# Kernel tuning notes

Measured on AMD Instinct MI355X. Metric: run time of the kernel, lower is better.

## Reference

```python
import jax, jax.numpy as jnp
import numpy as np

N_NODES = 100000
N_EDGES = 1600000
NUM_FEATURES = 128
HIDDEN_DIM = 64
NUM_CLASSES = 2
NUM_GRAPHS = 128


def setup_inputs() -> dict:
    key = jax.random.key(0)
    ks = jax.random.split(key, 9)
    x = jax.random.normal(ks[0], (N_NODES, NUM_FEATURES), dtype=jnp.float32)
    edge_index = jax.random.randint(ks[1], (2, N_EDGES), 0, N_NODES, dtype=jnp.int64)
    batch = jnp.sort(jax.random.randint(ks[2], (N_NODES,), 0, NUM_GRAPHS, dtype=jnp.int64))
    # GCNConv weights (PyG: glorot-init linear, zero bias; values here arbitrary for a numeric baseline)
    s1 = 1.0 / np.sqrt(NUM_FEATURES)
    s2 = 1.0 / np.sqrt(HIDDEN_DIM)
    W1 = jax.random.uniform(ks[3], (NUM_FEATURES, HIDDEN_DIM), jnp.float32, -s1, s1)
    b1 = jax.random.uniform(ks[4], (HIDDEN_DIM,), jnp.float32, -s1, s1)
    W2 = jax.random.uniform(ks[5], (HIDDEN_DIM, HIDDEN_DIM), jnp.float32, -s2, s2)
    b2 = jax.random.uniform(ks[6], (HIDDEN_DIM,), jnp.float32, -s2, s2)
    Wf = jax.random.uniform(ks[7], (HIDDEN_DIM, NUM_CLASSES), jnp.float32, -s2, s2)
    bf = jax.random.uniform(ks[8], (NUM_CLASSES,), jnp.float32, -s2, s2)
    return {"x": x, "edge_index": edge_index, "batch": batch,
            "W1": W1, "b1": b1, "W2": W2, "b2": b2, "Wf": Wf, "bf": bf}


def _gcn_aggregate(h, src, dst, norm, n_nodes):
    # messages: gather source features, scale by sym-norm coefficient, scatter-add at targets
    msg = h[src] * norm[:, None]                       # [E+N, F]
    return jax.ops.segment_sum(msg, dst, num_segments=n_nodes)


def reference(x, edge_index, batch, W1, b1, W2, b2, Wf, bf):
    n = x.shape[0]
    loops = jnp.arange(n, dtype=edge_index.dtype)
    # GCNConv adds self-loops and uses symmetric normalization D^{-1/2}(A+I)D^{-1/2}
    src = jnp.concatenate([edge_index[0], loops])
    dst = jnp.concatenate([edge_index[1], loops])
    deg = jax.ops.segment_sum(jnp.ones_like(dst, dtype=x.dtype), dst, num_segments=n)
    dis = jnp.where(deg > 0, jax.lax.rsqrt(jnp.maximum(deg, 1.0)), 0.0)
    norm = dis[src] * dis[dst]                         # per-edge coefficient

    h = jax.nn.relu(_gcn_aggregate(x @ W1, src, dst, norm, n) + b1)
    h = jax.nn.relu(_gcn_aggregate(h @ W2, src, dst, norm, n) + b2)

    # global_mean_pool over batch segment ids
    sums = jax.ops.segment_sum(h, batch, num_segments=NUM_GRAPHS)
    counts = jax.ops.segment_sum(jnp.ones((n,), dtype=h.dtype), batch, num_segments=NUM_GRAPHS)
    pooled = sums / jnp.maximum(counts, 1.0)[:, None]  # [G, hidden]

    return pooled @ Wf + bf                            # [G, num_classes]
```

## Files before the change

kernel.cpp:

```cpp
#include <hip/hip_runtime.h>
#include <hip/hip_bf16.h>


constexpr int F_IN   = 128;
constexpr int HID    = 64;
constexpr int NGRAPH = 128;
constexpr int NCLS   = 2;

constexpr int EPB = 4096;
constexpr int NB  = 391;
constexpr int DPB = 256;
constexpr int ST  = 56;

typedef __attribute__((ext_vector_type(8))) short bf16x8;
typedef __attribute__((ext_vector_type(4))) float f32x4;

__device__ __forceinline__ float bf2f(unsigned short s) {
    union { unsigned u; float f; } v; v.u = ((unsigned)s) << 16; return v.f;
}
__device__ __forceinline__ unsigned short f2bf(float f) {
    union { float f; unsigned u; } v; v.f = f;
    unsigned u = v.u;
    return (unsigned short)((u + 0x7FFFu + ((u >> 16) & 1u)) >> 16);
}
__device__ __forceinline__ void unpack8(uint4 g, float* f) {
    union { unsigned u; float x; } v;
    v.u = g.x << 16; f[0] = v.x;  v.u = g.x & 0xFFFF0000u; f[1] = v.x;
    v.u = g.y << 16; f[2] = v.x;  v.u = g.y & 0xFFFF0000u; f[3] = v.x;
    v.u = g.z << 16; f[4] = v.x;  v.u = g.z & 0xFFFF0000u; f[5] = v.x;
    v.u = g.w << 16; f[6] = v.x;  v.u = g.w & 0xFFFF0000u; f[7] = v.x;
}

__global__ __launch_bounds__(256) void k_bin2(const int* __restrict__ srcv,
                                              const int* __restrict__ dstv,
                                              int* __restrict__ gcur,
                                              unsigned* __restrict__ bin,
                                              int E, int cap) {
    __shared__ int h[NB];
    __shared__ int base[NB];
    __shared__ int ld[EPB];
    __shared__ int ls[EPB];
    for (int i = threadIdx.x; i < NB; i += 256) h[i] = 0;
    __syncthreads();
    int e0 = blockIdx.x * EPB, e1 = min(e0 + EPB, E), n = e1 - e0;
    for (int i = threadIdx.x; i < n; i += 256) {
        int d = dstv[e0 + i], s = srcv[e0 + i];
        ld[i] = d; ls[i] = s;
        atomicAdd(&h[d >> 8], 1);
    }
    __syncthreads();
    for (int i = threadIdx.x; i < NB; i += 256) {
        int c = h[i];
        base[i] = (c > 0) ? atomicAdd(&gcur[i], c) : 0;
        h[i] = 0;
    }
    __syncthreads();
    for (int i = threadIdx.x; i < n; i += 256) {
        int d = ld[i], s = ls[i];
        int b = d >> 8;
        int pos = base[b] + atomicAdd(&h[b], 1);
        bin[(size_t)b * cap + pos] = ((unsigned)(d & 255) << 20) | (unsigned)s;
    }
}

__global__ __launch_bounds__(256) void k_ell(const unsigned* __restrict__ bin,
                                             const int* __restrict__ bktCnt,
                                             int* __restrict__ ellg,
                                             int* __restrict__ cntg,
                                             float* __restrict__ disg,
                                             int N, int cap) {
    __shared__ int lcnt[DPB];
    __shared__ int lell[DPB * ST];
    int b = blockIdx.x;
    for (int i = threadIdx.x; i < DPB; i += 256) lcnt[i] = 0;
    for (int i = threadIdx.x; i < DPB * ST; i += 256) lell[i] = -1;
    __syncthreads();
    int n = bktCnt[b];
    const unsigned* src = bin + (size_t)b * cap;
    for (int i = threadIdx.x; i < n; i += 256) {
        unsigned p = src[i];
        int d = (int)(p >> 20);
        int s = (int)(p & 0xFFFFF);
        int pos = atomicAdd(&lcnt[d], 1);
        if (pos < ST) lell[d * ST + pos] = s;
    }
    __syncthreads();
    int base = b * DPB;
    int lim = (N - base) * ST;
    if (lim > DPB * ST) lim = DPB * ST;
    int* dst = ellg + (size_t)base * ST;
    for (int i = threadIdx.x; i < lim; i += 256) dst[i] = lell[i];
    for (int i = threadIdx.x; i < DPB; i += 256) {
        int r = base + i;
        if (r < N) {
            int c = min(lcnt[i], ST);
            cntg[r] = c;
            disg[r] = rsqrtf((float)c + 1.0f);
        }
    }
}

__global__ __launch_bounds__(256) void k_gemm_f(const float* __restrict__ X,
                                                const float* __restrict__ W,
                                                unsigned short* __restrict__ Y,
                                                int M) {
    constexpr int SRX = 136;
    constexpr int SRW = 136;
    __shared__ unsigned short Xs[128 * SRX];
    __shared__ unsigned short Wt[64 * SRW];
    const int t = threadIdx.x;
    const int row0 = blockIdx.x * 128;

#pragma unroll
    for (int i = 0; i < 16; ++i) {
        int idx = i * 256 + t;
        int r = idx >> 5, c4 = idx & 31;
        int gr = row0 + r;
        float4 v = (gr < M) ? *(const float4*)&X[(size_t)gr * 128 + c4 * 4]
                            : float4{0.f, 0.f, 0.f, 0.f};
        uint2 p{f2bf(v.x) | ((unsigned)f2bf(v.y) << 16),
                f2bf(v.z) | ((unsigned)f2bf(v.w) << 16)};
        *(uint2*)&Xs[r * SRX + c4 * 4] = p;
    }
#pragma unroll
    for (int i = 0; i < 8; ++i) {
        int idx = i * 256 + t;
        int k = idx >> 4, n4 = idx & 15;
        float4 v = *(const float4*)&W[(size_t)k * 64 + n4 * 4];
        Wt[(n4 * 4 + 0) * SRW + k] = f2bf(v.x);
        Wt[(n4 * 4 + 1) * SRW + k] = f2bf(v.y);
        Wt[(n4 * 4 + 2) * SRW + k] = f2bf(v.z);
        Wt[(n4 * 4 + 3) * SRW + k] = f2bf(v.w);
    }
    __syncthreads();

    const int ln = t & 63, wv = t >> 6;
    const int m16 = ln & 15, kg = ln >> 4;
    const int rbase = wv * 32;
    f32x4 acc[2][4];
#pragma unroll
    for (int i = 0; i < 2; ++i)
#pragma unroll
        for (int j = 0; j < 4; ++j) acc[i][j] = f32x4{0.f, 0.f, 0.f, 0.f};

#pragma unroll
    for (int ks = 0; ks < 4; ++ks) {
        bf16x8 a0 = *(const bf16x8*)&Xs[(rbase + m16) * SRX + ks * 32 + kg * 8];
        bf16x8 a1 = *(const bf16x8*)&Xs[(rbase + 16 + m16) * SRX + ks * 32 + kg * 8];
#pragma unroll
        for (int ct = 0; ct < 4; ++ct) {
            bf16x8 b = *(const bf16x8*)&Wt[(ct * 16 + m16) * SRW + ks * 32 + kg * 8];
            acc[0][ct] = __builtin_amdgcn_mfma_f32_16x16x32_bf16(a0, b, acc[0][ct], 0, 0, 0);
            acc[1][ct] = __builtin_amdgcn_mfma_f32_16x16x32_bf16(a1, b, acc[1][ct], 0, 0, 0);
        }
    }

    __syncthreads();
    unsigned short* Cs = Xs;
#pragma unroll
    for (int mt = 0; mt < 2; ++mt)
#pragma unroll
        for (int ct = 0; ct < 4; ++ct)
#pragma unroll
            for (int reg = 0; reg < 4; ++reg) {
                int r = rbase + mt * 16 + kg * 4 + reg;
                Cs[r * 64 + ct * 16 + m16] = f2bf(acc[mt][ct][reg]);
            }
    __syncthreads();
#pragma unroll
    for (int i = 0; i < 4; ++i) {
        int idx = i * 256 + t;
        int r = idx >> 3, c8 = idx & 7;
        int gr = row0 + r;
        if (gr < M)
            *(uint4*)&Y[(size_t)gr * 64 + c8 * 8] = *(const uint4*)&Cs[r * 64 + c8 * 8];
    }
}

__global__ __launch_bounds__(256) void k_gemm_b(const unsigned short* __restrict__ X,
                                                const float* __restrict__ W,
                                                unsigned short* __restrict__ Y,
                                                int M) {
    constexpr int SRX = 72;
    constexpr int SRW = 72;
    __shared__ unsigned short Xs[128 * SRX];
    __shared__ unsigned short Wt[64 * SRW];
    const int t = threadIdx.x;
    const int row0 = blockIdx.x * 128;

#pragma unroll
    for (int i = 0; i < 4; ++i) {
        int idx = i * 256 + t;
        int r = idx >> 3, c8 = idx & 7;
        int gr = row0 + r;
        uint4 v = (gr < M) ? *(const uint4*)&X[(size_t)gr * 64 + c8 * 8]
                           : uint4{0u, 0u, 0u, 0u};
        *(uint4*)&Xs[r * SRX + c8 * 8] = v;
    }
#pragma unroll
    for (int i = 0; i < 4; ++i) {
        int idx = i * 256 + t;
        int k = idx >> 4, n4 = idx & 15;
        float4 v = *(const float4*)&W[(size_t)k * 64 + n4 * 4];
        Wt[(n4 * 4 + 0) * SRW + k] = f2bf(v.x);
        Wt[(n4 * 4 + 1) * SRW + k] = f2bf(v.y);
        Wt[(n4 * 4 + 2) * SRW + k] = f2bf(v.z);
        Wt[(n4 * 4 + 3) * SRW + k] = f2bf(v.w);
    }
    __syncthreads();

    const int ln = t & 63, wv = t >> 6;
    const int m16 = ln & 15, kg = ln >> 4;
    const int rbase = wv * 32;
    f32x4 acc[2][4];
#pragma unroll
    for (int i = 0; i < 2; ++i)
#pragma unroll
        for (int j = 0; j < 4; ++j) acc[i][j] = f32x4{0.f, 0.f, 0.f, 0.f};

#pragma unroll
    for (int ks = 0; ks < 2; ++ks) {
        bf16x8 a0 = *(const bf16x8*)&Xs[(rbase + m16) * SRX + ks * 32 + kg * 8];
        bf16x8 a1 = *(const bf16x8*)&Xs[(rbase + 16 + m16) * SRX + ks * 32 + kg * 8];
#pragma unroll
        for (int ct = 0; ct < 4; ++ct) {
            bf16x8 b = *(const bf16x8*)&Wt[(ct * 16 + m16) * SRW + ks * 32 + kg * 8];
            acc[0][ct] = __builtin_amdgcn_mfma_f32_16x16x32_bf16(a0, b, acc[0][ct], 0, 0, 0);
            acc[1][ct] = __builtin_amdgcn_mfma_f32_16x16x32_bf16(a1, b, acc[1][ct], 0, 0, 0);
        }
    }

    __syncthreads();
    unsigned short* Cs = Xs;
#pragma unroll
    for (int mt = 0; mt < 2; ++mt)
#pragma unroll
        for (int ct = 0; ct < 4; ++ct)
#pragma unroll
            for (int reg = 0; reg < 4; ++reg) {
                int r = rbase + mt * 16 + kg * 4 + reg;
                Cs[r * 64 + ct * 16 + m16] = f2bf(acc[mt][ct][reg]);
            }
    __syncthreads();
#pragma unroll
    for (int i = 0; i < 4; ++i) {
        int idx = i * 256 + t;
        int r = idx >> 3, c8 = idx & 7;
        int gr = row0 + r;
        if (gr < M)
            *(uint4*)&Y[(size_t)gr * 64 + c8 * 8] = *(const uint4*)&Cs[r * 64 + c8 * 8];
    }
}

__global__ __launch_bounds__(256) void k_gather(const unsigned short* __restrict__ h,
                                                const int* __restrict__ ell,
                                                const int* __restrict__ cnt,
                                                const float* __restrict__ dis,
                                                const float* __restrict__ b,
                                                unsigned short* __restrict__ outb,
                                                int N) {
    int wave = (blockIdx.x * 256 + threadIdx.x) >> 6;
    int lane = threadIdx.x & 63;
    int nq   = lane >> 3;
    int sl   = lane & 7;
    int node = wave * 8 + nq;
    bool valid = node < N;
    int nc = valid ? node : N - 1;

    int deg  = cnt[nc];
    int degP = (deg + 7) & ~7;
    float dd = dis[nc];
    const uint4* h4 = (const uint4*)h;

    float acc[8], tmp[8];
    unpack8(h4[(size_t)nc * 8 + sl], acc);
    float sw = dd * dd;
    float4 bv0 = *(const float4*)&b[sl * 8];
    float4 bv1 = *(const float4*)&b[sl * 8 + 4];
    acc[0] = acc[0] * sw + bv0.x; acc[1] = acc[1] * sw + bv0.y;
    acc[2] = acc[2] * sw + bv0.z; acc[3] = acc[3] * sw + bv0.w;
    acc[4] = acc[4] * sw + bv1.x; acc[5] = acc[5] * sw + bv1.y;
    acc[6] = acc[6] * sw + bv1.z; acc[7] = acc[7] * sw + bv1.w;

    for (int j0 = 0; j0 < degP; j0 += 8) {
        int raw = ell[(size_t)nc * ST + j0 + sl];
        int   idx = (raw >= 0) ? raw : 0;
        float w   = (raw >= 0) ? dis[idx] * dd : 0.f;
#pragma unroll
        for (int jj = 0; jj < 8; ++jj) {
            int   s  = __shfl(idx, nq * 8 + jj, 64);
            float wj = __shfl(w,   nq * 8 + jj, 64);
            uint4 g = h4[(size_t)s * 8 + sl];
            unpack8(g, tmp);
#pragma unroll
            for (int q = 0; q < 8; ++q)
                acc[q] = fmaf(tmp[q], wj, acc[q]);
        }
    }
    if (valid) {
        uint4 p;
        p.x = f2bf(fmaxf(acc[0], 0.f)) | ((unsigned)f2bf(fmaxf(acc[1], 0.f)) << 16);
        p.y = f2bf(fmaxf(acc[2], 0.f)) | ((unsigned)f2bf(fmaxf(acc[3], 0.f)) << 16);
        p.z = f2bf(fmaxf(acc[4], 0.f)) | ((unsigned)f2bf(fmaxf(acc[5], 0.f)) << 16);
        p.w = f2bf(fmaxf(acc[6], 0.f)) | ((unsigned)f2bf(fmaxf(acc[7], 0.f)) << 16);
        ((uint4*)outb)[(size_t)node * 8 + sl] = p;
    }
}

constexpr int POOL_CHUNK = 16;
__global__ __launch_bounds__(256) void k_pool(const unsigned short* __restrict__ h,
                                              const int* __restrict__ batch,
                                              float* __restrict__ sums,
                                              float* __restrict__ gcnt, int N) {
    int wave = (blockIdx.x * 256 + threadIdx.x) >> 6;
    int lane = threadIdx.x & 63;
    int n0 = wave * POOL_CHUNK;
    if (n0 >= N) return;
    int n1 = min(n0 + POOL_CHUNK, N);

    int   gcur = batch[n0];
    float acc  = 0.f;
    int   run  = 0;
    for (int n = n0; n < n1; ++n) {
        int g = batch[n];
        if (g != gcur) {
            atomicAdd(&sums[gcur * HID + lane], acc);
            if (lane == 0) atomicAdd(&gcnt[gcur], (float)run);
            gcur = g; acc = 0.f; run = 0;
        }
        acc += bf2f(h[(size_t)n * HID + lane]);
        ++run;
    }
    atomicAdd(&sums[gcur * HID + lane], acc);
    if (lane == 0) atomicAdd(&gcnt[gcur], (float)run);
}

__global__ __launch_bounds__(256) void k_final(const float* __restrict__ sums,
                                               const float* __restrict__ gcnt,
                                               const float* __restrict__ Wf,
                                               const float* __restrict__ bfv,
                                               float* __restrict__ out) {
    int t = threadIdx.x;
    int g = t >> 1, c = t & 1;
    float invc = 1.0f / fmaxf(gcnt[g], 1.0f);
    float acc = bfv[c];
#pragma unroll
    for (int k = 0; k < HID; ++k)
        acc = fmaf(sums[g * HID + k] * invc, Wf[k * NCLS + c], acc);
    out[g * NCLS + c] = acc;
}

extern "C" void kernel_launch(void* const* d_in, const int* in_sizes, int n_in,
                              void* d_out, int out_size, void* d_ws, size_t ws_size,
                              hipStream_t stream) {
    const float* x   = (const float*)d_in[0];
    const int*   ei  = (const int*)d_in[1];
    const int*   bat = (const int*)d_in[2];
    const float* W1  = (const float*)d_in[3];
    const float* b1  = (const float*)d_in[4];
    const float* W2  = (const float*)d_in[5];
    const float* b2  = (const float*)d_in[6];
    const float* Wf  = (const float*)d_in[7];
    const float* bfv = (const float*)d_in[8];
    float* out = (float*)d_out;

    const int N = in_sizes[0] / F_IN;
    const int E = in_sizes[1] / 2;
    const int* srcv = ei;
    const int* dstv = ei + E;

    const int nblk = (E + EPB - 1) / EPB;
    const int cap  = E / NB + 1280;

    const size_t S2 = (size_t)N * HID * 2;
    char* ws = (char*)d_ws;
    unsigned short* bufA = (unsigned short*)ws;
    unsigned short* bufB = (unsigned short*)(ws + S2);
    int*   ell  = (int*)(ws + 2 * S2);
    char*  tail = ws + 2 * S2 + (size_t)N * ST * 4;
    int*   cnt  = (int*)tail;
    float* dis  = (float*)(tail + (size_t)N * 4);
    float* sums = (float*)(tail + (size_t)N * 8);
    float* gcnt = sums + NGRAPH * HID;
    int*   gcur = (int*)(gcnt + NGRAPH);

    unsigned* bin = (unsigned*)bufA;

    hipMemsetAsync(sums, 0, (size_t)(NGRAPH * HID + NGRAPH + NB) * 4, stream);

    k_bin2<<<nblk, 256, 0, stream>>>(srcv, dstv, gcur, bin, E, cap);
    k_ell<<<NB, 256, 0, stream>>>(bin, gcur, ell, cnt, dis, N, cap);

    const int gemmBlk = (N + 127) / 128;
    const int gathBlk = (N + 31) / 32;
    k_gemm_f<<<gemmBlk, 256, 0, stream>>>(x, W1, bufA, N);
    k_gather<<<gathBlk, 256, 0, stream>>>(bufA, ell, cnt, dis, b1, bufB, N);

    k_gemm_b<<<gemmBlk, 256, 0, stream>>>(bufB, W2, bufA, N);
    k_gather<<<gathBlk, 256, 0, stream>>>(bufA, ell, cnt, dis, b2, bufB, N);

    const int poolBlk = (((N + POOL_CHUNK - 1) / POOL_CHUNK) + 3) / 4;
    k_pool<<<poolBlk, 256, 0, stream>>>(bufB, bat, sums, gcnt, N);
    k_final<<<1, 256, 0, stream>>>(sums, gcnt, Wf, bfv, out);
}
```

Before: 259.7 us.

## Merge first GEMM with edge binning and fuse pooling with final classifier

The first feature GEMM and the edge-binning pass now run as a single horizontally fused launch, split by block index and sharing one shared-memory buffer, so the two independent stages overlap on the GPU. The bin buffer moves out of bufA into the workspace tail because the GEMM now writes bufA at the same time. Mean pooling is rewritten as one block per graph: each block binary-searches the sorted batch vector for its node range, reduces with shuffles and shared memory, and applies the classifier directly. This drops the atomics, the memset of the sums and the separate final kernel, at the cost of only 128 pooling blocks and uneven per-block work.

```diff
diff --git a/kernel.cpp b/kernel.cpp
--- a/kernel.cpp
+++ b/kernel.cpp
@@ -31,35 +31,117 @@
     v.u = g.w << 16; f[6] = v.x;  v.u = g.w & 0xFFFF0000u; f[7] = v.x;
 }
 
-__global__ __launch_bounds__(256) void k_bin2(const int* __restrict__ srcv,
-                                              const int* __restrict__ dstv,
-                                              int* __restrict__ gcur,
-                                              unsigned* __restrict__ bin,
-                                              int E, int cap) {
-    __shared__ int h[NB];
-    __shared__ int base[NB];
-    __shared__ int ld[EPB];
-    __shared__ int ls[EPB];
-    for (int i = threadIdx.x; i < NB; i += 256) h[i] = 0;
-    __syncthreads();
-    int e0 = blockIdx.x * EPB, e1 = min(e0 + EPB, E), n = e1 - e0;
-    for (int i = threadIdx.x; i < n; i += 256) {
-        int d = dstv[e0 + i], s = srcv[e0 + i];
-        ld[i] = d; ls[i] = s;
-        atomicAdd(&h[d >> 8], 1);
-    }
-    __syncthreads();
-    for (int i = threadIdx.x; i < NB; i += 256) {
-        int c = h[i];
-        base[i] = (c > 0) ? atomicAdd(&gcur[i], c) : 0;
-        h[i] = 0;
-    }
-    __syncthreads();
-    for (int i = threadIdx.x; i < n; i += 256) {
-        int d = ld[i], s = ls[i];
-        int b = d >> 8;
-        int pos = base[b] + atomicAdd(&h[b], 1);
-        bin[(size_t)b * cap + pos] = ((unsigned)(d & 255) << 20) | (unsigned)s;
+__global__ __launch_bounds__(256) void k_pre(const float* __restrict__ X,
+                                             const float* __restrict__ W,
+                                             unsigned short* __restrict__ Y,
+                                             int M,
+                                             const int* __restrict__ srcv,
+                                             const int* __restrict__ dstv,
+                                             int* __restrict__ gcur,
+                                             unsigned* __restrict__ bin,
+                                             int E, int cap, int gemmBlk) {
+    __shared__ __align__(16) char smem[52224];
+    const int t = threadIdx.x;
+
+    if ((int)blockIdx.x < gemmBlk) {
+        constexpr int SRX = 136;
+        constexpr int SRW = 136;
+        unsigned short* Xs = (unsigned short*)smem;
+        unsigned short* Wt = (unsigned short*)(smem + 34816);
+        const int row0 = blockIdx.x * 128;
+
+#pragma unroll
+        for (int i = 0; i < 16; ++i) {
+            int idx = i * 256 + t;
+            int r = idx >> 5, c4 = idx & 31;
+            int gr = row0 + r;
+            float4 v = (gr < M) ? *(const float4*)&X[(size_t)gr * 128 + c4 * 4]
+                                : float4{0.f, 0.f, 0.f, 0.f};
+            uint2 p{f2bf(v.x) | ((unsigned)f2bf(v.y) << 16),
+                    f2bf(v.z) | ((unsigned)f2bf(v.w) << 16)};
+            *(uint2*)&Xs[r * SRX + c4 * 4] = p;
+        }
+#pragma unroll
+        for (int i = 0; i < 8; ++i) {
+            int idx = i * 256 + t;
+            int k = idx >> 4, n4 = idx & 15;
+            float4 v = *(const float4*)&W[(size_t)k * 64 + n4 * 4];
+            Wt[(n4 * 4 + 0) * SRW + k] = f2bf(v.x);
+            Wt[(n4 * 4 + 1) * SRW + k] = f2bf(v.y);
+            Wt[(n4 * 4 + 2) * SRW + k] = f2bf(v.z);
+            Wt[(n4 * 4 + 3) * SRW + k] = f2bf(v.w);
+        }
+        __syncthreads();
+
+        const int ln = t & 63, wv = t >> 6;
+        const int m16 = ln & 15, kg = ln >> 4;
+        const int rbase = wv * 32;
+        f32x4 acc[2][4];
+#pragma unroll
+        for (int i = 0; i < 2; ++i)
+#pragma unroll
+            for (int j = 0; j < 4; ++j) acc[i][j] = f32x4{0.f, 0.f, 0.f, 0.f};
+
+#pragma unroll
+        for (int ks = 0; ks < 4; ++ks) {
+            bf16x8 a0 = *(const bf16x8*)&Xs[(rbase + m16) * SRX + ks * 32 + kg * 8];
+            bf16x8 a1 = *(const bf16x8*)&Xs[(rbase + 16 + m16) * SRX + ks * 32 + kg * 8];
+#pragma unroll
+            for (int ct = 0; ct < 4; ++ct) {
+                bf16x8 b = *(const bf16x8*)&Wt[(ct * 16 + m16) * SRW + ks * 32 + kg * 8];
+                acc[0][ct] = __builtin_amdgcn_mfma_f32_16x16x32_bf16(a0, b, acc[0][ct], 0, 0, 0);
+                acc[1][ct] = __builtin_amdgcn_mfma_f32_16x16x32_bf16(a1, b, acc[1][ct], 0, 0, 0);
+            }
+        }
+
+        __syncthreads();
+        unsigned short* Cs = Xs;
+#pragma unroll
+        for (int mt = 0; mt < 2; ++mt)
+#pragma unroll
+            for (int ct = 0; ct < 4; ++ct)
+#pragma unroll
+                for (int reg = 0; reg < 4; ++reg) {
+                    int r = rbase + mt * 16 + kg * 4 + reg;
+                    Cs[r * 64 + ct * 16 + m16] = f2bf(acc[mt][ct][reg]);
+                }
+        __syncthreads();
+#pragma unroll
+        for (int i = 0; i < 4; ++i) {
+            int idx = i * 256 + t;
+            int r = idx >> 3, c8 = idx & 7;
+            int gr = row0 + r;
+            if (gr < M)
+                *(uint4*)&Y[(size_t)gr * 64 + c8 * 8] = *(const uint4*)&Cs[r * 64 + c8 * 8];
+        }
+    } else {
+        int* h    = (int*)smem;
+        int* base = h + NB;
+        int* ld   = base + NB;
+        int* ls   = ld + EPB;
+        const int bb = blockIdx.x - gemmBlk;
+
+        for (int i = t; i < NB; i += 256) h[i] = 0;
+        __syncthreads();
+        int e0 = bb * EPB, e1 = min(e0 + EPB, E), n = e1 - e0;
+        for (int i = t; i < n; i += 256) {
+            int d = dstv[e0 + i], s = srcv[e0 + i];
+            ld[i] = d; ls[i] = s;
+            atomicAdd(&h[d >> 8], 1);
+        }
+        __syncthreads();
+        for (int i = t; i < NB; i += 256) {
+            int c = h[i];
+            base[i] = (c > 0) ? atomicAdd(&gcur[i], c) : 0;
+            h[i] = 0;
+        }
+        __syncthreads();
+        for (int i = t; i < n; i += 256) {
+            int d = ld[i], s = ls[i];
+            int b = d >> 8;
+            int pos = base[b] + atomicAdd(&h[b], 1);
+            bin[(size_t)b * cap + pos] = ((unsigned)(d & 255) << 20) | (unsigned)s;
+        }
     }
 }
 
@@ -97,83 +179,6 @@
             cntg[r] = c;
             disg[r] = rsqrtf((float)c + 1.0f);
         }
-    }
-}
-
-__global__ __launch_bounds__(256) void k_gemm_f(const float* __restrict__ X,
-                                                const float* __restrict__ W,
-                                                unsigned short* __restrict__ Y,
-                                                int M) {
-    constexpr int SRX = 136;
-    constexpr int SRW = 136;
-    __shared__ unsigned short Xs[128 * SRX];
-    __shared__ unsigned short Wt[64 * SRW];
-    const int t = threadIdx.x;
-    const int row0 = blockIdx.x * 128;
-
-#pragma unroll
-    for (int i = 0; i < 16; ++i) {
-        int idx = i * 256 + t;
-        int r = idx >> 5, c4 = idx & 31;
-        int gr = row0 + r;
-        float4 v = (gr < M) ? *(const float4*)&X[(size_t)gr * 128 + c4 * 4]
-                            : float4{0.f, 0.f, 0.f, 0.f};
-        uint2 p{f2bf(v.x) | ((unsigned)f2bf(v.y) << 16),
-                f2bf(v.z) | ((unsigned)f2bf(v.w) << 16)};
-        *(uint2*)&Xs[r * SRX + c4 * 4] = p;
-    }
-#pragma unroll
-    for (int i = 0; i < 8; ++i) {
-        int idx = i * 256 + t;
-        int k = idx >> 4, n4 = idx & 15;
-        float4 v = *(const float4*)&W[(size_t)k * 64 + n4 * 4];
-        Wt[(n4 * 4 + 0) * SRW + k] = f2bf(v.x);
-        Wt[(n4 * 4 + 1) * SRW + k] = f2bf(v.y);
-        Wt[(n4 * 4 + 2) * SRW + k] = f2bf(v.z);
-        Wt[(n4 * 4 + 3) * SRW + k] = f2bf(v.w);
-    }
-    __syncthreads();
-
-    const int ln = t & 63, wv = t >> 6;
-    const int m16 = ln & 15, kg = ln >> 4;
-    const int rbase = wv * 32;
-    f32x4 acc[2][4];
-#pragma unroll
-    for (int i = 0; i < 2; ++i)
-#pragma unroll
-        for (int j = 0; j < 4; ++j) acc[i][j] = f32x4{0.f, 0.f, 0.f, 0.f};
-
-#pragma unroll
-    for (int ks = 0; ks < 4; ++ks) {
-        bf16x8 a0 = *(const bf16x8*)&Xs[(rbase + m16) * SRX + ks * 32 + kg * 8];
-        bf16x8 a1 = *(const bf16x8*)&Xs[(rbase + 16 + m16) * SRX + ks * 32 + kg * 8];
-#pragma unroll
-        for (int ct = 0; ct < 4; ++ct) {
-            bf16x8 b = *(const bf16x8*)&Wt[(ct * 16 + m16) * SRW + ks * 32 + kg * 8];
-            acc[0][ct] = __builtin_amdgcn_mfma_f32_16x16x32_bf16(a0, b, acc[0][ct], 0, 0, 0);
-            acc[1][ct] = __builtin_amdgcn_mfma_f32_16x16x32_bf16(a1, b, acc[1][ct], 0, 0, 0);
-        }
-    }
-
-    __syncthreads();
-    unsigned short* Cs = Xs;
-#pragma unroll
-    for (int mt = 0; mt < 2; ++mt)
-#pragma unroll
-        for (int ct = 0; ct < 4; ++ct)
-#pragma unroll
-            for (int reg = 0; reg < 4; ++reg) {
-                int r = rbase + mt * 16 + kg * 4 + reg;
-                Cs[r * 64 + ct * 16 + m16] = f2bf(acc[mt][ct][reg]);
-            }
-    __syncthreads();
-#pragma unroll
-    for (int i = 0; i < 4; ++i) {
-        int idx = i * 256 + t;
-        int r = idx >> 3, c8 = idx & 7;
-        int gr = row0 + r;
-        if (gr < M)
-            *(uint4*)&Y[(size_t)gr * 64 + c8 * 8] = *(const uint4*)&Cs[r * 64 + c8 * 8];
     }
 }
 
@@ -307,47 +312,59 @@
     }
 }
 
-constexpr int POOL_CHUNK = 16;
-__global__ __launch_bounds__(256) void k_pool(const unsigned short* __restrict__ h,
-                                              const int* __restrict__ batch,
-                                              float* __restrict__ sums,
-                                              float* __restrict__ gcnt, int N) {
-    int wave = (blockIdx.x * 256 + threadIdx.x) >> 6;
-    int lane = threadIdx.x & 63;
-    int n0 = wave * POOL_CHUNK;
-    if (n0 >= N) return;
-    int n1 = min(n0 + POOL_CHUNK, N);
-
-    int   gcur = batch[n0];
-    float acc  = 0.f;
-    int   run  = 0;
-    for (int n = n0; n < n1; ++n) {
-        int g = batch[n];
-        if (g != gcur) {
-            atomicAdd(&sums[gcur * HID + lane], acc);
-            if (lane == 0) atomicAdd(&gcnt[gcur], (float)run);
-            gcur = g; acc = 0.f; run = 0;
-        }
-        acc += bf2f(h[(size_t)n * HID + lane]);
-        ++run;
-    }
-    atomicAdd(&sums[gcur * HID + lane], acc);
-    if (lane == 0) atomicAdd(&gcnt[gcur], (float)run);
-}
-
-__global__ __launch_bounds__(256) void k_final(const float* __restrict__ sums,
-                                               const float* __restrict__ gcnt,
+__global__ __launch_bounds__(256) void k_pool2(const unsigned short* __restrict__ h,
+                                               const int* __restrict__ batch,
                                                const float* __restrict__ Wf,
                                                const float* __restrict__ bfv,
-                                               float* __restrict__ out) {
-    int t = threadIdx.x;
-    int g = t >> 1, c = t & 1;
-    float invc = 1.0f / fmaxf(gcnt[g], 1.0f);
-    float acc = bfv[c];
-#pragma unroll
-    for (int k = 0; k < HID; ++k)
-        acc = fmaf(sums[g * HID + k] * invc, Wf[k * NCLS + c], acc);
-    out[g * NCLS + c] = acc;
+                                               float* __restrict__ out, int N) {
+    __shared__ float part[4 * 64];
+    const int g = blockIdx.x;
+    const int t = threadIdx.x;
+
+    int lo = 0, hi = N;
+    while (lo < hi) { int mid = (lo + hi) >> 1; if (batch[mid] < g) lo = mid + 1; else hi = mid; }
+    const int start = lo;
+    hi = N;
+    while (lo < hi) { int mid = (lo + hi) >> 1; if (batch[mid] < g + 1) lo = mid + 1; else hi = mid; }
+    const int end = lo;
+
+    const int sl = t & 7;
+    const int ns = t >> 3;
+    const uint4* h4 = (const uint4*)h;
+    float acc[8], tmp[8];
+#pragma unroll
+    for (int q = 0; q < 8; ++q) acc[q] = 0.f;
+    for (int n = start + ns; n < end; n += 32) {
+        unpack8(h4[(size_t)n * 8 + sl], tmp);
+#pragma unroll
+        for (int q = 0; q < 8; ++q) acc[q] += tmp[q];
+    }
+#pragma unroll
+    for (int m = 8; m <= 32; m <<= 1)
+#pragma unroll
+        for (int q = 0; q < 8; ++q) acc[q] += __shfl_xor(acc[q], m, 64);
+    const int lane = t & 63, w = t >> 6;
+    if ((lane >> 3) == 0) {
+#pragma unroll
+        for (int q = 0; q < 8; ++q) part[w * 64 + sl * 8 + q] = acc[q];
+    }
+    __syncthreads();
+    if (w == 0) {
+        float tot = part[lane] + part[64 + lane] + part[128 + lane] + part[192 + lane];
+        float invc = 1.0f / fmaxf((float)(end - start), 1.0f);
+        float p = tot * invc;
+        float c0 = p * Wf[lane * NCLS + 0];
+        float c1 = p * Wf[lane * NCLS + 1];
+#pragma unroll
+        for (int m = 32; m >= 1; m >>= 1) {
+            c0 += __shfl_xor(c0, m, 64);
+            c1 += __shfl_xor(c1, m, 64);
+        }
+        if (lane == 0) {
+            out[g * NCLS + 0] = c0 + bfv[0];
+            out[g * NCLS + 1] = c1 + bfv[1];
+        }
+    }
 }
 
 extern "C" void kernel_launch(void* const* d_in, const int* in_sizes, int n_in,
@@ -380,26 +397,21 @@
     char*  tail = ws + 2 * S2 + (size_t)N * ST * 4;
     int*   cnt  = (int*)tail;
     float* dis  = (float*)(tail + (size_t)N * 4);
-    float* sums = (float*)(tail + (size_t)N * 8);
-    float* gcnt = sums + NGRAPH * HID;
-    int*   gcur = (int*)(gcnt + NGRAPH);
-
-    unsigned* bin = (unsigned*)bufA;
-
-    hipMemsetAsync(sums, 0, (size_t)(NGRAPH * HID + NGRAPH + NB) * 4, stream);
-
-    k_bin2<<<nblk, 256, 0, stream>>>(srcv, dstv, gcur, bin, E, cap);
+    int*   gcur = (int*)(tail + (size_t)N * 8);
+    unsigned* bin = (unsigned*)(tail + (size_t)N * 8 + 4096);
+
+    hipMemsetAsync(gcur, 0, (size_t)NB * 4, stream);
+
+    const int gemmBlk = (N + 127) / 128;
+    k_pre<<<gemmBlk + nblk, 256, 0, stream>>>(x, W1, bufA, N, srcv, dstv,
+                                              gcur, bin, E, cap, gemmBlk);
     k_ell<<<NB, 256, 0, stream>>>(bin, gcur, ell, cnt, dis, N, cap);
 
-    const int gemmBlk = (N + 127) / 128;
     const int gathBlk = (N + 31) / 32;
-    k_gemm_f<<<gemmBlk, 256, 0, stream>>>(x, W1, bufA, N);
     k_gather<<<gathBlk, 256, 0, stream>>>(bufA, ell, cnt, dis, b1, bufB, N);
 
     k_gemm_b<<<gemmBlk, 256, 0, stream>>>(bufB, W2, bufA, N);
     k_gather<<<gathBlk, 256, 0, stream>>>(bufA, ell, cnt, dis, b2, bufB, N);
 
-    const int poolBlk = (((N + POOL_CHUNK - 1) / POOL_CHUNK) + 3) / 4;
-    k_pool<<<poolBlk, 256, 0, stream>>>(bufB, bat, sums, gcnt, N);
-    k_final<<<1, 256, 0, stream>>>(sums, gcnt, Wf, bfv, out);
-}
+    k_pool2<<<NGRAPH, 256, 0, stream>>>(bufB, bat, Wf, bfv, out, N);
+}
```

Result: faster. 240.2 us (-7.5%).
